# Kernel tuning notes

Hardware: AMD Instinct MI355X
Metric: run time of the kernel (lower is better)

## Reference

```python
import jax, jax.numpy as jnp
import numpy as np
import math

B = 16
D = 1024
K = 64
ALPHA = 0.0
N_MAX = 8192


def setup_inputs() -> dict:
    key = jax.random.key(0)
    k1, k2 = jax.random.split(key)
    lengths = jax.random.randint(k1, (B,), N_MAX // 2, N_MAX + 1)
    lengths = lengths.at[0].set(N_MAX)  # ensure max(lengths) == N_MAX, matching torch N_max
    lengths = lengths.astype(jnp.int64) if jax.config.jax_enable_x64 else lengths.astype(jnp.int32)
    W = jax.random.normal(k2, (D, 2 * K), dtype=jnp.float32) * (1.0 / math.sqrt(2 * K))
    return {"lengths": lengths, "W": W, "N_max": N_MAX}


def reference(lengths, W, N_max):
    # lengths: [B] int, W: [d, 2K] (torch Linear weight), N_max: python int
    d, twoK = W.shape
    Kk = twoK // 2
    k = jnp.arange(1, Kk + 1, dtype=jnp.float32)                      # [K]
    Delta = 2.0 * math.pi * k[None, :] / lengths[:, None].astype(jnp.float32)  # [B, K]
    t = jnp.arange(N_max, dtype=jnp.float32)                          # [N]
    theta = t[None, :, None] * Delta[:, None, :]                      # [B, N, K] closed-form angle
    amp = (k ** (-ALPHA)) * (1.0 / math.sqrt(Kk))                     # [K]
    # interleave (cos, sin) pairs along last dim: [c1,s1,c2,s2,...]
    cs = jnp.stack([jnp.cos(theta), jnp.sin(theta)], axis=-1)         # [B, N, K, 2]
    feats = (cs * amp[None, None, :, None]).reshape(theta.shape[0], N_max, twoK)
    mask = jnp.arange(N_max)[None, :] < lengths[:, None]              # [B, N]
    feats = feats * mask[:, :, None].astype(feats.dtype)
    pos_emb = jnp.einsum('bnf,df->bnd', feats, W)                     # [B, N, d]
    return pos_emb, mask
```

## Files before the change

kernel.cpp:

```cpp
#include <hip/hip_runtime.h>
#include <math.h>

#define B_DIM    16
#define D_DIM    1024
#define K_FREQ   64
#define F_DIM    128
#define N_MAXLEN 8192

#define BM   128
#define BN   128
#define LDSS 136
#define TILE_SHORTS (128 * LDSS)
#define A_CHUNKS 2176
#define ALL_CHUNKS (2 * A_CHUNKS)

typedef __attribute__((ext_vector_type(8))) short bf16x8;
typedef __attribute__((ext_vector_type(4))) float f32x4;

__device__ __forceinline__ unsigned f2bf(float x) {
    union { float f; unsigned u; } v; v.f = x;
    return (v.u + 0x7FFFu + ((v.u >> 16) & 1u)) >> 16;
}

__device__ __forceinline__ void gload_lds16(const void* g, void* l) {
    __builtin_amdgcn_global_load_lds(
        (const __attribute__((address_space(1))) void*)g,
        (__attribute__((address_space(3))) void*)l, 16, 0, 0);
}

__global__ __launch_bounds__(256) void prep_w_kernel(
    const int* __restrict__ lengths,
    const float* __restrict__ W,
    short* __restrict__ Wb,
    float* __restrict__ maskp)
{
    const int i = blockIdx.x * 256 + threadIdx.x;
    const float4 w = ((const float4*)W)[i];
    const int row = i >> 5;
    const int c4  = i & 31;
    uint2 packed;
    packed.x = f2bf(w.x) | (f2bf(w.y) << 16);
    packed.y = f2bf(w.z) | (f2bf(w.w) << 16);
    *(uint2*)&Wb[(size_t)row * LDSS + c4 * 4] = packed;

    const int m4  = i << 2;
    const int b   = m4 >> 13;
    const int n   = m4 & (N_MAXLEN - 1);
    const int len = lengths[b];
    float4 mv;
    mv.x = (n     < len) ? 1.f : 0.f;
    mv.y = (n + 1 < len) ? 1.f : 0.f;
    mv.z = (n + 2 < len) ? 1.f : 0.f;
    mv.w = (n + 3 < len) ? 1.f : 0.f;
    ((float4*)maskp)[i] = mv;
}

__global__ __launch_bounds__(256) void feats_kernel(
    const int* __restrict__ lengths,
    short* __restrict__ Wf)
{
    const int g    = blockIdx.x * 256 + threadIdx.x;
    const int m    = g >> 1;
    const int half = g & 1;
    const int b    = m >> 13;
    const int n    = m & (N_MAXLEN - 1);
    const int len  = lengths[b];

    unsigned vals[32];
    if (n >= len) {
        #pragma unroll
        for (int j = 0; j < 32; ++j) vals[j] = 0u;
    } else {
        const float base = (float)n / (float)len;
        #pragma unroll
        for (int j = 0; j < 32; ++j) {
            const int k = half * 32 + j;
            float rev = base * (float)(k + 1);
            rev -= floorf(rev);
            float s, c;
            __sincosf(6.283185307179586f * rev, &s, &c);
            vals[j] = f2bf(c * 0.125f) | (f2bf(s * 0.125f) << 16);
        }
    }
    uint4* dst = (uint4*)&Wf[(size_t)m * LDSS + half * 64];
    #pragma unroll
    for (int i = 0; i < 8; ++i)
        dst[i] = (uint4){vals[4*i], vals[4*i+1], vals[4*i+2], vals[4*i+3]};
}

__global__ __launch_bounds__(256, 2) void cyclic_gemm_kernel(
    const int* __restrict__ lengths,
    const short* __restrict__ Wb,
    const short* __restrict__ Wf,
    float* __restrict__ out)
{
    __shared__ short s[2 * TILE_SHORTS];

    const int tid = threadIdx.x;
    const int m0  = blockIdx.x * BM;
    const int d0  = blockIdx.y * BN;
    const int b   = m0 >> 13;
    const int n0  = m0 & (N_MAXLEN - 1);
    const int len = lengths[b];

    if (n0 >= len) {
        const float4 z = {0.f, 0.f, 0.f, 0.f};
        #pragma unroll 4
        for (int i = tid; i < BM * BN / 4; i += 256) {
            const int r = i >> 5;
            const int c = i & 31;
            *(float4*)(out + (size_t)(m0 + r) * D_DIM + d0 + c * 4) = z;
        }
        return;
    }

    {
        const short* Af = Wf + (size_t)m0 * LDSS;
        const short* Bf = Wb + (size_t)d0 * LDSS;
        #pragma unroll
        for (int i = 0; i < 17; ++i) {
            const int chunk = i * 256 + tid;
            const short* src = (chunk < A_CHUNKS) ? (Af + (size_t)chunk * 8)
                                                  : (Bf + (size_t)(chunk - A_CHUNKS) * 8);
            gload_lds16(src, s + (size_t)chunk * 8);
        }
    }
    __syncthreads();

    const int lane = tid & 63;
    const int wave = tid >> 6;
    const int wm   = (wave >> 1) * 64;
    const int wn   = (wave & 1) * 64;
    const int lrow = lane & 15;
    const int quad = lane >> 4;

    f32x4 acc[4][4];
    #pragma unroll
    for (int mi = 0; mi < 4; ++mi)
        #pragma unroll
        for (int ni = 0; ni < 4; ++ni)
            acc[mi][ni] = (f32x4){0.f, 0.f, 0.f, 0.f};

    const short* aBase = &s[(wm + lrow) * LDSS + quad * 8];
    const short* bBase = &s[TILE_SHORTS + (wn + lrow) * LDSS + quad * 8];

    #pragma unroll
    for (int ks = 0; ks < 4; ++ks) {
        bf16x8 af[4], bfr[4];
        #pragma unroll
        for (int i = 0; i < 4; ++i) {
            af[i]  = *(const bf16x8*)(aBase + i * 16 * LDSS + ks * 32);
            bfr[i] = *(const bf16x8*)(bBase + i * 16 * LDSS + ks * 32);
        }
        #pragma unroll
        for (int mi = 0; mi < 4; ++mi)
            #pragma unroll
            for (int ni = 0; ni < 4; ++ni)
                acc[mi][ni] = __builtin_amdgcn_mfma_f32_16x16x32_bf16(
                    af[mi], bfr[ni], acc[mi][ni], 0, 0, 0);
    }

    #pragma unroll
    for (int mi = 0; mi < 4; ++mi) {
        #pragma unroll
        for (int reg = 0; reg < 4; ++reg) {
            const int row = m0 + wm + mi * 16 + quad * 4 + reg;
            float* orow = out + (size_t)row * D_DIM + (d0 + wn + lrow);
            #pragma unroll
            for (int ni = 0; ni < 4; ++ni)
                orow[ni * 16] = acc[mi][ni][reg];
        }
    }
}

extern "C" void kernel_launch(void* const* d_in, const int* in_sizes, int n_in,
                              void* d_out, int out_size, void* d_ws, size_t ws_size,
                              hipStream_t stream) {
    const int*   lengths = (const int*)d_in[0];
    const float* W       = (const float*)d_in[1];
    float* out   = (float*)d_out;
    float* maskp = out + (size_t)B_DIM * N_MAXLEN * D_DIM;

    const size_t wb_bytes = (size_t)D_DIM * LDSS * sizeof(short);
    const size_t wf_bytes = (size_t)B_DIM * N_MAXLEN * LDSS * sizeof(short);
    short* Wb;
    if (ws_size >= wb_bytes + wf_bytes) {
        Wb = (short*)d_ws;
    } else {
        Wb = (short*)(maskp + (size_t)B_DIM * N_MAXLEN);
    }
    short* Wf = Wb + (size_t)D_DIM * LDSS;

    prep_w_kernel<<<dim3(128), dim3(256), 0, stream>>>(lengths, W, Wb, maskp);
    feats_kernel<<<dim3((B_DIM * N_MAXLEN * 2) / 256), dim3(256), 0, stream>>>(lengths, Wf);

    dim3 grid((B_DIM * N_MAXLEN) / BM, D_DIM / BN);
    cyclic_gemm_kernel<<<grid, dim3(256), 0, stream>>>(lengths, Wb, Wf, out);
}
```

Before: 594.7 us.

## Fuse sinusoid feature generation into GEMM and switch to XOR-swizzled LDS layout

Removes the separate feats kernel and its global bf16 feature buffer. Each GEMM block now computes its 64-row feature tile directly into LDS with sincos, and the W tile is loaded with an XOR swizzle in place of padding. The tile shrinks to 64x128 with a launch bound of 3 blocks per CU, and the operands are swapped so each lane writes float4 output stores. The cost is recomputing the features once per column block (8 times per row), in exchange for skipping a roughly 36MB write and reread of features.

```diff
diff --git a/kernel.cpp b/kernel.cpp
--- a/kernel.cpp
+++ b/kernel.cpp
@@ -7,12 +7,8 @@
 #define F_DIM    128
 #define N_MAXLEN 8192
 
-#define BM   128
-#define BN   128
-#define LDSS 136
-#define TILE_SHORTS (128 * LDSS)
-#define A_CHUNKS 2176
-#define ALL_CHUNKS (2 * A_CHUNKS)
+#define BM 64
+#define BN 128
 
 typedef __attribute__((ext_vector_type(8))) short bf16x8;
 typedef __attribute__((ext_vector_type(4))) float f32x4;
@@ -37,11 +33,13 @@
     const int i = blockIdx.x * 256 + threadIdx.x;
     const float4 w = ((const float4*)W)[i];
     const int row = i >> 5;
-    const int c4  = i & 31;
-    uint2 packed;
-    packed.x = f2bf(w.x) | (f2bf(w.y) << 16);
-    packed.y = f2bf(w.z) | (f2bf(w.w) << 16);
-    *(uint2*)&Wb[(size_t)row * LDSS + c4 * 4] = packed;
+    const int o8  = i & 31;
+    const int c   = o8 >> 1;
+    const int sw  = c ^ (row & 7);
+    uint2 p;
+    p.x = f2bf(w.x) | (f2bf(w.y) << 16);
+    p.y = f2bf(w.z) | (f2bf(w.w) << 16);
+    *(uint2*)((char*)Wb + (size_t)row * 256 + sw * 16 + (o8 & 1) * 8) = p;
 
     const int m4  = i << 2;
     const int b   = m4 >> 13;
@@ -55,46 +53,13 @@
     ((float4*)maskp)[i] = mv;
 }
 
-__global__ __launch_bounds__(256) void feats_kernel(
-    const int* __restrict__ lengths,
-    short* __restrict__ Wf)
-{
-    const int g    = blockIdx.x * 256 + threadIdx.x;
-    const int m    = g >> 1;
-    const int half = g & 1;
-    const int b    = m >> 13;
-    const int n    = m & (N_MAXLEN - 1);
-    const int len  = lengths[b];
-
-    unsigned vals[32];
-    if (n >= len) {
-        #pragma unroll
-        for (int j = 0; j < 32; ++j) vals[j] = 0u;
-    } else {
-        const float base = (float)n / (float)len;
-        #pragma unroll
-        for (int j = 0; j < 32; ++j) {
-            const int k = half * 32 + j;
-            float rev = base * (float)(k + 1);
-            rev -= floorf(rev);
-            float s, c;
-            __sincosf(6.283185307179586f * rev, &s, &c);
-            vals[j] = f2bf(c * 0.125f) | (f2bf(s * 0.125f) << 16);
-        }
-    }
-    uint4* dst = (uint4*)&Wf[(size_t)m * LDSS + half * 64];
-    #pragma unroll
-    for (int i = 0; i < 8; ++i)
-        dst[i] = (uint4){vals[4*i], vals[4*i+1], vals[4*i+2], vals[4*i+3]};
-}
-
-__global__ __launch_bounds__(256, 2) void cyclic_gemm_kernel(
+__global__ __launch_bounds__(256, 3) void cyclic_gemm_kernel(
     const int* __restrict__ lengths,
     const short* __restrict__ Wb,
-    const short* __restrict__ Wf,
     float* __restrict__ out)
 {
-    __shared__ short s[2 * TILE_SHORTS];
+    __shared__ short sA[BM * 128];
+    __shared__ short sB[BN * 128];
 
     const int tid = threadIdx.x;
     const int m0  = blockIdx.x * BM;
@@ -105,71 +70,101 @@
 
     if (n0 >= len) {
         const float4 z = {0.f, 0.f, 0.f, 0.f};
-        #pragma unroll 4
-        for (int i = tid; i < BM * BN / 4; i += 256) {
-            const int r = i >> 5;
-            const int c = i & 31;
+        #pragma unroll
+        for (int i = 0; i < 8; ++i) {
+            const int lin = i * 256 + tid;
+            const int r = lin >> 5;
+            const int c = lin & 31;
             *(float4*)(out + (size_t)(m0 + r) * D_DIM + d0 + c * 4) = z;
         }
         return;
     }
 
     {
-        const short* Af = Wf + (size_t)m0 * LDSS;
-        const short* Bf = Wb + (size_t)d0 * LDSS;
+        const char* src = (const char*)Wb + (size_t)d0 * 256;
         #pragma unroll
-        for (int i = 0; i < 17; ++i) {
+        for (int i = 0; i < 8; ++i) {
             const int chunk = i * 256 + tid;
-            const short* src = (chunk < A_CHUNKS) ? (Af + (size_t)chunk * 8)
-                                                  : (Bf + (size_t)(chunk - A_CHUNKS) * 8);
-            gload_lds16(src, s + (size_t)chunk * 8);
+            gload_lds16(src + (size_t)chunk * 16, (char*)sB + (size_t)chunk * 16);
+        }
+    }
+
+    {
+        const int r   = tid >> 2;
+        const int q4  = tid & 3;
+        const int n   = n0 + r;
+        const int swz = r & 7;
+        char* rowbase = (char*)sA + r * 256;
+        if (n >= len) {
+            const uint4 z = {0u, 0u, 0u, 0u};
+            #pragma unroll
+            for (int cc = 0; cc < 4; ++cc)
+                *(uint4*)(rowbase + ((q4 * 4 + cc) ^ swz) * 16) = z;
+        } else {
+            const float base = (float)n / (float)len;
+            #pragma unroll
+            for (int cc = 0; cc < 4; ++cc) {
+                unsigned v[4];
+                #pragma unroll
+                for (int j = 0; j < 4; ++j) {
+                    const int k = q4 * 16 + cc * 4 + j;
+                    float rev = base * (float)(k + 1);
+                    rev -= floorf(rev);
+                    float s, c;
+                    __sincosf(6.283185307179586f * rev, &s, &c);
+                    v[j] = f2bf(c * 0.125f) | (f2bf(s * 0.125f) << 16);
+                }
+                *(uint4*)(rowbase + ((q4 * 4 + cc) ^ swz) * 16) =
+                    (uint4){v[0], v[1], v[2], v[3]};
+            }
         }
     }
     __syncthreads();
 
     const int lane = tid & 63;
     const int wave = tid >> 6;
-    const int wm   = (wave >> 1) * 64;
+    const int wm   = (wave >> 1) * 32;
     const int wn   = (wave & 1) * 64;
     const int lrow = lane & 15;
     const int quad = lane >> 4;
 
-    f32x4 acc[4][4];
+    f32x4 acc[2][4];
     #pragma unroll
-    for (int mi = 0; mi < 4; ++mi)
+    for (int mi = 0; mi < 2; ++mi)
         #pragma unroll
         for (int ni = 0; ni < 4; ++ni)
             acc[mi][ni] = (f32x4){0.f, 0.f, 0.f, 0.f};
 
-    const short* aBase = &s[(wm + lrow) * LDSS + quad * 8];
-    const short* bBase = &s[TILE_SHORTS + (wn + lrow) * LDSS + quad * 8];
-
     #pragma unroll
     for (int ks = 0; ks < 4; ++ks) {
-        bf16x8 af[4], bfr[4];
+        bf16x8 wf[4], ff[2];
         #pragma unroll
-        for (int i = 0; i < 4; ++i) {
-            af[i]  = *(const bf16x8*)(aBase + i * 16 * LDSS + ks * 32);
-            bfr[i] = *(const bf16x8*)(bBase + i * 16 * LDSS + ks * 32);
+        for (int ni = 0; ni < 4; ++ni) {
+            const int rr = wn + ni * 16 + lrow;
+            wf[ni] = *(const bf16x8*)((const char*)sB + rr * 256 +
+                        ((ks * 64 + quad * 16) ^ ((rr & 7) << 4)));
         }
         #pragma unroll
-        for (int mi = 0; mi < 4; ++mi)
+        for (int mi = 0; mi < 2; ++mi) {
+            const int rr = wm + mi * 16 + lrow;
+            ff[mi] = *(const bf16x8*)((const char*)sA + rr * 256 +
+                        ((ks * 64 + quad * 16) ^ ((rr & 7) << 4)));
+        }
+        #pragma unroll
+        for (int mi = 0; mi < 2; ++mi)
             #pragma unroll
             for (int ni = 0; ni < 4; ++ni)
                 acc[mi][ni] = __builtin_amdgcn_mfma_f32_16x16x32_bf16(
-                    af[mi], bfr[ni], acc[mi][ni], 0, 0, 0);
+                    wf[ni], ff[mi], acc[mi][ni], 0, 0, 0);
     }
 
     #pragma unroll
-    for (int mi = 0; mi < 4; ++mi) {
+    for (int mi = 0; mi < 2; ++mi) {
+        const int m = m0 + wm + mi * 16 + lrow;
+        float* orow = out + (size_t)m * D_DIM + d0 + wn + quad * 4;
         #pragma unroll
-        for (int reg = 0; reg < 4; ++reg) {
-            const int row = m0 + wm + mi * 16 + quad * 4 + reg;
-            float* orow = out + (size_t)row * D_DIM + (d0 + wn + lrow);
-            #pragma unroll
-            for (int ni = 0; ni < 4; ++ni)
-                orow[ni * 16] = acc[mi][ni][reg];
-        }
+        for (int ni = 0; ni < 4; ++ni)
+            *(float4*)(orow + ni * 16) = *(float4*)&acc[mi][ni];
     }
 }
 
@@ -181,19 +176,16 @@
     float* out   = (float*)d_out;
     float* maskp = out + (size_t)B_DIM * N_MAXLEN * D_DIM;
 
-    const size_t wb_bytes = (size_t)D_DIM * LDSS * sizeof(short);
-    const size_t wf_bytes = (size_t)B_DIM * N_MAXLEN * LDSS * sizeof(short);
+    const size_t wb_bytes = (size_t)D_DIM * F_DIM * sizeof(short);
     short* Wb;
-    if (ws_size >= wb_bytes + wf_bytes) {
+    if (ws_size >= wb_bytes) {
         Wb = (short*)d_ws;
     } else {
         Wb = (short*)(maskp + (size_t)B_DIM * N_MAXLEN);
     }
-    short* Wf = Wb + (size_t)D_DIM * LDSS;
 
     prep_w_kernel<<<dim3(128), dim3(256), 0, stream>>>(lengths, W, Wb, maskp);
-    feats_kernel<<<dim3((B_DIM * N_MAXLEN * 2) / 256), dim3(256), 0, stream>>>(lengths, Wf);
 
     dim3 grid((B_DIM * N_MAXLEN) / BM, D_DIM / BN);
-    cyclic_gemm_kernel<<<grid, dim3(256), 0, stream>>>(lengths, Wb, Wf, out);
+    cyclic_gemm_kernel<<<grid, dim3(256), 0, stream>>>(lengths, Wb, out);
 }
```

After: 558.6 us. -6.1%, faster.

## Fuse sinusoid feature generation into GEMM and vectorize output stores

Applied to the files above, without the earlier changes.

Drops the separate feats kernel and its large bf16 feature buffer in global memory. Each GEMM block now computes its 128-row sin/cos feature tile directly into LDS while the W tile streams in asynchronously. The MFMA operands are swapped so each lane holds four contiguous output columns and can write float4 stores, and the grid is transposed so blocks sharing a feature tile run next to each other. The cost is that the transcendentals are recomputed once for each of the 8 column blocks that share a row tile.

```diff
diff --git a/kernel.cpp b/kernel.cpp
--- a/kernel.cpp
+++ b/kernel.cpp
@@ -11,8 +11,6 @@
 #define BN   128
 #define LDSS 136
 #define TILE_SHORTS (128 * LDSS)
-#define A_CHUNKS 2176
-#define ALL_CHUNKS (2 * A_CHUNKS)
 
 typedef __attribute__((ext_vector_type(8))) short bf16x8;
 typedef __attribute__((ext_vector_type(4))) float f32x4;
@@ -55,80 +53,78 @@
     ((float4*)maskp)[i] = mv;
 }
 
-__global__ __launch_bounds__(256) void feats_kernel(
-    const int* __restrict__ lengths,
-    short* __restrict__ Wf)
-{
-    const int g    = blockIdx.x * 256 + threadIdx.x;
-    const int m    = g >> 1;
-    const int half = g & 1;
-    const int b    = m >> 13;
-    const int n    = m & (N_MAXLEN - 1);
-    const int len  = lengths[b];
-
-    unsigned vals[32];
-    if (n >= len) {
-        #pragma unroll
-        for (int j = 0; j < 32; ++j) vals[j] = 0u;
-    } else {
-        const float base = (float)n / (float)len;
-        #pragma unroll
-        for (int j = 0; j < 32; ++j) {
-            const int k = half * 32 + j;
-            float rev = base * (float)(k + 1);
-            rev -= floorf(rev);
-            float s, c;
-            __sincosf(6.283185307179586f * rev, &s, &c);
-            vals[j] = f2bf(c * 0.125f) | (f2bf(s * 0.125f) << 16);
-        }
-    }
-    uint4* dst = (uint4*)&Wf[(size_t)m * LDSS + half * 64];
-    #pragma unroll
-    for (int i = 0; i < 8; ++i)
-        dst[i] = (uint4){vals[4*i], vals[4*i+1], vals[4*i+2], vals[4*i+3]};
-}
-
 __global__ __launch_bounds__(256, 2) void cyclic_gemm_kernel(
     const int* __restrict__ lengths,
     const short* __restrict__ Wb,
-    const short* __restrict__ Wf,
     float* __restrict__ out)
 {
-    __shared__ short s[2 * TILE_SHORTS];
+    __shared__ short sA[TILE_SHORTS];
+    __shared__ short sB[TILE_SHORTS];
 
     const int tid = threadIdx.x;
-    const int m0  = blockIdx.x * BM;
-    const int d0  = blockIdx.y * BN;
+    const int m0  = blockIdx.y * BM;
+    const int d0  = blockIdx.x * BN;
     const int b   = m0 >> 13;
     const int n0  = m0 & (N_MAXLEN - 1);
     const int len = lengths[b];
+    const int lane = tid & 63;
+    const int wave = tid >> 6;
 
     if (n0 >= len) {
         const float4 z = {0.f, 0.f, 0.f, 0.f};
-        #pragma unroll 4
-        for (int i = tid; i < BM * BN / 4; i += 256) {
-            const int r = i >> 5;
-            const int c = i & 31;
+        #pragma unroll
+        for (int i = 0; i < 8; ++i) {
+            const int lin = i * 256 + tid;
+            const int r = lin >> 5;
+            const int c = lin & 31;
             *(float4*)(out + (size_t)(m0 + r) * D_DIM + d0 + c * 4) = z;
         }
         return;
     }
 
     {
-        const short* Af = Wf + (size_t)m0 * LDSS;
         const short* Bf = Wb + (size_t)d0 * LDSS;
         #pragma unroll
-        for (int i = 0; i < 17; ++i) {
-            const int chunk = i * 256 + tid;
-            const short* src = (chunk < A_CHUNKS) ? (Af + (size_t)chunk * 8)
-                                                  : (Bf + (size_t)(chunk - A_CHUNKS) * 8);
-            gload_lds16(src, s + (size_t)chunk * 8);
+        for (int i = 0; i < 8; ++i) {
+            const int chunk = i * 256 + wave * 64 + lane;
+            gload_lds16(Bf + (size_t)chunk * 8, sB + (size_t)chunk * 8);
+        }
+        if (wave < 2) {
+            const int chunk = 2048 + wave * 64 + lane;
+            gload_lds16(Bf + (size_t)chunk * 8, sB + (size_t)chunk * 8);
         }
     }
+
+    {
+        const int r    = tid >> 1;
+        const int half = tid & 1;
+        const int n    = n0 + r;
+        uint4* dst = (uint4*)&sA[r * LDSS + half * 64];
+        if (n >= len) {
+            const uint4 z = {0u, 0u, 0u, 0u};
+            #pragma unroll
+            for (int g = 0; g < 8; ++g) dst[g] = z;
+        } else {
+            const float base = (float)n / (float)len;
+            #pragma unroll
+            for (int g = 0; g < 8; ++g) {
+                unsigned v[4];
+                #pragma unroll
+                for (int j = 0; j < 4; ++j) {
+                    const int k = half * 32 + g * 4 + j;
+                    float rev = base * (float)(k + 1);
+                    rev -= floorf(rev);
+                    float s, c;
+                    __sincosf(6.283185307179586f * rev, &s, &c);
+                    v[j] = f2bf(c * 0.125f) | (f2bf(s * 0.125f) << 16);
+                }
+                dst[g] = (uint4){v[0], v[1], v[2], v[3]};
+            }
+        }
+    }
+
     __syncthreads();
 
-    const int lane = tid & 63;
-    const int wave = tid >> 6;
     const int wm   = (wave >> 1) * 64;
     const int wn   = (wave & 1) * 64;
     const int lrow = lane & 15;
@@ -141,8 +137,8 @@
         for (int ni = 0; ni < 4; ++ni)
             acc[mi][ni] = (f32x4){0.f, 0.f, 0.f, 0.f};
 
-    const short* aBase = &s[(wm + lrow) * LDSS + quad * 8];
-    const short* bBase = &s[TILE_SHORTS + (wn + lrow) * LDSS + quad * 8];
+    const short* aBase = &sA[(wm + lrow) * LDSS + quad * 8];
+    const short* bBase = &sB[(wn + lrow) * LDSS + quad * 8];
 
     #pragma unroll
     for (int ks = 0; ks < 4; ++ks) {
@@ -157,19 +153,16 @@
             #pragma unroll
             for (int ni = 0; ni < 4; ++ni)
                 acc[mi][ni] = __builtin_amdgcn_mfma_f32_16x16x32_bf16(
-                    af[mi], bfr[ni], acc[mi][ni], 0, 0, 0);
+                    bfr[ni], af[mi], acc[mi][ni], 0, 0, 0);
     }
 
     #pragma unroll
     for (int mi = 0; mi < 4; ++mi) {
+        const int m = m0 + wm + mi * 16 + lrow;
+        float* orow = out + (size_t)m * D_DIM + d0 + wn + quad * 4;
         #pragma unroll
-        for (int reg = 0; reg < 4; ++reg) {
-            const int row = m0 + wm + mi * 16 + quad * 4 + reg;
-            float* orow = out + (size_t)row * D_DIM + (d0 + wn + lrow);
-            #pragma unroll
-            for (int ni = 0; ni < 4; ++ni)
-                orow[ni * 16] = acc[mi][ni][reg];
-        }
+        for (int ni = 0; ni < 4; ++ni)
+            *(float4*)(orow + ni * 16) = *(float4*)&acc[mi][ni];
     }
 }
 
@@ -182,18 +175,15 @@
     float* maskp = out + (size_t)B_DIM * N_MAXLEN * D_DIM;
 
     const size_t wb_bytes = (size_t)D_DIM * LDSS * sizeof(short);
-    const size_t wf_bytes = (size_t)B_DIM * N_MAXLEN * LDSS * sizeof(short);
     short* Wb;
-    if (ws_size >= wb_bytes + wf_bytes) {
+    if (ws_size >= wb_bytes) {
         Wb = (short*)d_ws;
     } else {
         Wb = (short*)(maskp + (size_t)B_DIM * N_MAXLEN);
     }
-    short* Wf = Wb + (size_t)D_DIM * LDSS;
 
     prep_w_kernel<<<dim3(128), dim3(256), 0, stream>>>(lengths, W, Wb, maskp);
-    feats_kernel<<<dim3((B_DIM * N_MAXLEN * 2) / 256), dim3(256), 0, stream>>>(lengths, Wf);
 
-    dim3 grid((B_DIM * N_MAXLEN) / BM, D_DIM / BN);
-    cyclic_gemm_kernel<<<grid, dim3(256), 0, stream>>>(lengths, Wb, Wf, out);
+    dim3 grid(D_DIM / BN, (B_DIM * N_MAXLEN) / BM);
+    cyclic_gemm_kernel<<<grid, dim3(256), 0, stream>>>(lengths, Wb, out);
 }
```

Measured after the change: 524.1 us. 1.13x faster.
